# Kernel tuning notes

Hardware: AMD Instinct MI355X
Metric: run time of the kernel (lower is better)

Reference implementation:

```python
import jax, jax.numpy as jnp
import numpy as np

WH, WW = 14, 14
NUM_HEADS = 12
NUM_REL = (2 * WH - 1) * (2 * WW - 1) + 3  # 732


def _gen_rel_pos_index(wh, ww):
    # Faithful numpy port of gen_relative_position_index (static, host-side)
    area = wh * ww
    coords = np.stack(np.meshgrid(np.arange(wh), np.arange(ww), indexing='ij'))  # (2, wh, ww)
    cf = coords.reshape(2, -1)  # (2, area)
    rel = cf[:, :, None] - cf[:, None, :]  # (2, area, area)
    rel = rel.transpose(1, 2, 0).copy()  # (area, area, 2)
    rel[..., 0] += wh - 1
    rel[..., 1] += ww - 1
    rel[..., 0] *= 2 * ww - 1
    nrd = (2 * wh - 1) * (2 * ww - 1) + 3
    idx = np.zeros((area + 1, area + 1), dtype=np.int64)
    idx[1:, 1:] = rel.sum(-1)
    idx[0, 0:] = nrd - 3
    idx[0:, 0] = nrd - 2
    idx[0, 0] = nrd - 1
    return idx


REL_IDX = jnp.asarray(_gen_rel_pos_index(WH, WW))  # (197, 197) int


def setup_inputs() -> dict:
    key = jax.random.key(0)
    k0, k1, k2, k3 = jax.random.split(key, 4)
    B, N, C = 64, WH * WW + 1, 768
    x = jax.random.normal(k0, (B, N, C), jnp.float32)
    qkv_w = jax.random.normal(k1, (3 * C, C), jnp.float32) * 0.02
    q_bias = jnp.zeros((C,), jnp.float32)
    k_bias = jnp.zeros((C,), jnp.float32)  # non-trainable buffer, always zeros
    v_bias = jnp.zeros((C,), jnp.float32)
    rel_table = jax.random.normal(k2, (NUM_REL, NUM_HEADS), jnp.float32) * 0.02
    proj_w = jax.random.normal(k3, (C, C), jnp.float32) * 0.02
    proj_b = jnp.zeros((C,), jnp.float32)
    return {"x": x, "qkv_w": qkv_w, "q_bias": q_bias, "k_bias": k_bias,
            "v_bias": v_bias, "rel_table": rel_table, "proj_w": proj_w, "proj_b": proj_b}


def reference(x, qkv_w, q_bias, k_bias, v_bias, rel_table, proj_w, proj_b):
    B, N, C = x.shape
    H = NUM_HEADS
    D = C // H
    scale = D ** -0.5
    # fused qkv projection with concatenated (q, k(zero), v) bias
    qkv_bias = jnp.concatenate([q_bias, k_bias, v_bias])
    qkv = x @ qkv_w.T + qkv_bias  # (B, N, 3C)
    qkv = qkv.reshape(B, N, 3, H, D).transpose(2, 0, 3, 1, 4)  # (3, B, H, N, D)
    q, k, v = qkv[0], qkv[1], qkv[2]
    # scores + gathered relative position bias
    attn = jnp.einsum('bhnd,bhmd->bhnm', q * scale, k)  # (B, H, N, N)
    rpb = rel_table[REL_IDX].transpose(2, 0, 1)  # (H, N, N)
    attn = jax.nn.softmax(attn + rpb[None], axis=-1)
    out = jnp.einsum('bhnm,bhmd->bhnd', attn, v)  # (B, H, N, D)
    out = out.transpose(0, 2, 1, 3).reshape(B, N, C)
    return out @ proj_w.T + proj_b
```

## Files before the change

kernel.cpp:

```cpp
#include <hip/hip_runtime.h>
#include <math.h>

#define B_   64
#define N_   197
#define C_   768
#define H_   12
#define D_   64
#define BN   12608
#define BN_PAD 12672
#define QKV_ELEMS 9682944
#define SCALE 0.125f
#define STRV 80

typedef unsigned short ushort_t;
using bf16x8  = __attribute__((ext_vector_type(8))) __bf16;
using floatx4 = __attribute__((ext_vector_type(4))) float;
using ushort8 = __attribute__((ext_vector_type(8))) unsigned short;

__device__ __forceinline__ ushort_t f2bf(float f) {
    union { float f; unsigned u; } v; v.f = f;
    unsigned r = v.u + 0x7FFF + ((v.u >> 16) & 1);
    return (ushort_t)(r >> 16);
}

__device__ __forceinline__ void gload_lds16(const void* g, void* l) {
    __builtin_amdgcn_global_load_lds(
        (const __attribute__((address_space(1))) unsigned*)g,
        (__attribute__((address_space(3))) unsigned*)l, 16, 0, 0);
}

__global__ __launch_bounds__(256) void cvt_f32_bf16(
    const float* __restrict__ src, ushort_t* __restrict__ dst, int n4)
{
    int i = blockIdx.x * 256 + threadIdx.x;
    if (i < n4) {
        float4 v = ((const float4*)src)[i];
        ushort4 o;
        o.x = f2bf(v.x); o.y = f2bf(v.y); o.z = f2bf(v.z); o.w = f2bf(v.w);
        ((ushort4*)dst)[i] = o;
    }
}

__global__ __launch_bounds__(256, 4) void qkv_gemm_mfma(
    const ushort_t* __restrict__ xb,
    const ushort_t* __restrict__ wb,
    const float* __restrict__ qb,
    const float* __restrict__ kb,
    const float* __restrict__ vb,
    ushort_t* __restrict__ qkvb)
{
    __shared__ ushort_t lA[128 * 64];
    __shared__ ushort_t lB[128 * 64];
    const int t = threadIdx.x;
    const int w = t >> 6, lane = t & 63;
    const int quad = lane >> 4, li = lane & 15;
    const int wm = w >> 1, wn = w & 1;
    const int o0 = blockIdx.x * 128, m0 = blockIdx.y * 128;

    floatx4 acc[4][4];
#pragma unroll
    for (int i = 0; i < 4; ++i)
#pragma unroll
        for (int j = 0; j < 4; ++j) acc[i][j] = (floatx4)0.f;

    const int rloc = lane >> 3;
    const int gdma = (lane & 7) ^ rloc;
    const int rx   = li & 7;

    for (int kt = 0; kt < 12; ++kt) {
        const int k0 = kt * 64;
#pragma unroll
        for (int s = 0; s < 4; ++s) {
            const int rb = w * 32 + s * 8;
            gload_lds16(xb + ((size_t)(m0 + rb + rloc)) * 768 + k0 + gdma * 8,
                        &lA[rb * 64]);
            gload_lds16(wb + ((size_t)(o0 + rb + rloc)) * 768 + k0 + gdma * 8,
                        &lB[rb * 64]);
        }
        __syncthreads();
#pragma unroll
        for (int kk = 0; kk < 2; ++kk) {
            bf16x8 af[4], bfr[4];
#pragma unroll
            for (int mi = 0; mi < 4; ++mi)
                af[mi] = *(const bf16x8*)
                    &lA[(wm * 64 + mi * 16 + li) * 64 + ((kk * 4 + quad) ^ rx) * 8];
#pragma unroll
            for (int ni = 0; ni < 4; ++ni)
                bfr[ni] = *(const bf16x8*)
                    &lB[(wn * 64 + ni * 16 + li) * 64 + ((kk * 4 + quad) ^ rx) * 8];
#pragma unroll
            for (int mi = 0; mi < 4; ++mi)
#pragma unroll
                for (int ni = 0; ni < 4; ++ni)
                    acc[mi][ni] = __builtin_amdgcn_mfma_f32_16x16x32_bf16(
                        af[mi], bfr[ni], acc[mi][ni], 0, 0, 0);
        }
        __syncthreads();
    }

    const int which = o0 / 768;
    const float* bias = (which == 0) ? qb : ((which == 1) ? kb : vb);
    ushort_t* dst = qkvb + (size_t)which * QKV_ELEMS;
    const float sc = (which == 0) ? SCALE : 1.0f;

#pragma unroll
    for (int mi = 0; mi < 4; ++mi) {
#pragma unroll
        for (int r = 0; r < 4; ++r) {
            const int m = m0 + wm * 64 + mi * 16 + quad * 4 + r;
            if (m < BN) {
                const int b = m / 197, n = m % 197;
#pragma unroll
                for (int ni = 0; ni < 4; ++ni) {
                    const int o  = o0 + wn * 64 + ni * 16 + li;
                    const int ol = o - which * 768;
                    const int h = ol >> 6, d = ol & 63;
                    dst[(((size_t)b * 12 + h) * 197 + n) * 64 + d] =
                        f2bf((acc[mi][ni][r] + bias[ol]) * sc);
                }
            }
        }
    }
}

__global__ __launch_bounds__(256, 4) void attn_mfma(
    const ushort_t* __restrict__ qkvb,
    const float* __restrict__ rel_table,
    ushort_t* __restrict__ aout)
{
    __shared__ ushort_t Qs[64 * 64];
    __shared__ ushort_t Ks[64 * 64];
    __shared__ ushort_t Vt[64 * STRV];
    __shared__ ushort_t Ps[64 * STRV];
    __shared__ float relh[732];

    const int rt = blockIdx.x, bh = blockIdx.y;
    const int h = bh % 12, bb = bh / 12;
    const int t = threadIdx.x;
    const int w = t >> 6, lane = t & 63, quad = lane >> 4, li = lane & 15;
    const size_t base = (size_t)bh * (197 * 64);
    const ushort_t* Qg = qkvb + base;
    const ushort_t* Kg = qkvb + (size_t)QKV_ELEMS + base;
    const ushort_t* Vg = qkvb + (size_t)2 * QKV_ELEMS + base;
    const int r0 = rt * 64;

    for (int i = t; i < 732; i += 256) relh[i] = rel_table[i * 12 + h];

    {
        const int rloc = lane >> 3, g = (lane & 7) ^ rloc;
#pragma unroll
        for (int s = 0; s < 2; ++s) {
            const int rb = (w * 2 + s) * 8;
            gload_lds16(Qg + (size_t)(r0 + rb + rloc) * 64 + g * 8, &Qs[rb * 64]);
        }
    }

    int nrow[4], p14[4], pm[4];
#pragma unroll
    for (int r = 0; r < 4; ++r) {
        const int n = r0 + w * 16 + quad * 4 + r;
        nrow[r] = n;
        const int ne = (n < 197) ? n : 0;
        const int p = (ne > 0) ? ne - 1 : 0;
        p14[r] = p / 14; pm[r] = p % 14;
    }

    float m_run[4], l_run[4];
    floatx4 accO[4];
#pragma unroll
    for (int r = 0; r < 4; ++r) { m_run[r] = -INFINITY; l_run[r] = 0.f; }
#pragma unroll
    for (int dt = 0; dt < 4; ++dt) accO[dt] = (floatx4)0.f;

    __syncthreads();

    bf16x8 aq0, aq1;
    {
        const int rq = w * 16 + li, rxq = rq & 7;
        aq0 = *(const bf16x8*)&Qs[rq * 64 + (quad ^ rxq) * 8];
        aq1 = *(const bf16x8*)&Qs[rq * 64 + ((4 + quad) ^ rxq) * 8];
    }

    for (int cc = 0; cc < 4; ++cc) {
        {
            const int rloc = lane >> 3, g = (lane & 7) ^ rloc;
#pragma unroll
            for (int s = 0; s < 2; ++s) {
                const int rb = (w * 2 + s) * 8;
                gload_lds16(Kg + (size_t)(cc * 64 + rb + rloc) * 64 + g * 8,
                            &Ks[rb * 64]);
            }
        }
        {
            const int c = lane;
            const int mg = cc * 64 + c;
            ushort8 v0, v1;
            if (mg < 197) {
                v0 = *(const ushort8*)(Vg + (size_t)mg * 64 + w * 16);
                v1 = *(const ushort8*)(Vg + (size_t)mg * 64 + w * 16 + 8);
            } else {
                v0 = (ushort8)(unsigned short)0; v1 = v0;
            }
#pragma unroll
            for (int j = 0; j < 8; ++j) Vt[(w * 16 + j) * STRV + c] = v0[j];
#pragma unroll
            for (int j = 0; j < 8; ++j) Vt[(w * 16 + 8 + j) * STRV + c] = v1[j];
        }
        __syncthreads();

        floatx4 sacc[4];
#pragma unroll
        for (int tl = 0; tl < 4; ++tl) {
            const int rk = tl * 16 + li, rxk = rk & 7;
            bf16x8 bk0 = *(const bf16x8*)&Ks[rk * 64 + (quad ^ rxk) * 8];
            bf16x8 bk1 = *(const bf16x8*)&Ks[rk * 64 + ((4 + quad) ^ rxk) * 8];
            floatx4 sa = (floatx4)0.f;
            sa = __builtin_amdgcn_mfma_f32_16x16x32_bf16(aq0, bk0, sa, 0, 0, 0);
            sa = __builtin_amdgcn_mfma_f32_16x16x32_bf16(aq1, bk1, sa, 0, 0, 0);
            sacc[tl] = sa;
        }

#pragma unroll
        for (int tl = 0; tl < 4; ++tl) {
            const int mg = cc * 64 + tl * 16 + li;
            if (mg >= 197) {
#pragma unroll
                for (int r = 0; r < 4; ++r) sacc[tl][r] = -INFINITY;
            } else {
                const int qq = (mg > 0) ? mg - 1 : 0;
                const int q14 = qq / 14, qm = qq % 14;
#pragma unroll
                for (int r = 0; r < 4; ++r) {
                    int idx;
                    const int n0 = (nrow[r] < 197) ? nrow[r] : 0;
                    if (n0 == 0 && mg == 0)      idx = 731;
                    else if (n0 == 0)            idx = 729;
                    else if (mg == 0)            idx = 730;
                    else idx = (p14[r] - q14 + 13) * 27 + (pm[r] - qm + 13);
                    sacc[tl][r] += relh[idx];
                }
            }
        }

#pragma unroll
        for (int r = 0; r < 4; ++r) {
            float mx = fmaxf(fmaxf(sacc[0][r], sacc[1][r]),
                             fmaxf(sacc[2][r], sacc[3][r]));
            mx = fmaxf(mx, __shfl_xor(mx, 1));
            mx = fmaxf(mx, __shfl_xor(mx, 2));
            mx = fmaxf(mx, __shfl_xor(mx, 4));
            mx = fmaxf(mx, __shfl_xor(mx, 8));
            const float mnew = fmaxf(m_run[r], mx);
            const float alpha = __expf(m_run[r] - mnew);
            m_run[r] = mnew;
            const float p0 = __expf(sacc[0][r] - mnew);
            const float p1 = __expf(sacc[1][r] - mnew);
            const float p2 = __expf(sacc[2][r] - mnew);
            const float p3 = __expf(sacc[3][r] - mnew);
            float rs = p0 + p1 + p2 + p3;
            rs += __shfl_xor(rs, 1);
            rs += __shfl_xor(rs, 2);
            rs += __shfl_xor(rs, 4);
            rs += __shfl_xor(rs, 8);
            l_run[r] = l_run[r] * alpha + rs;
#pragma unroll
            for (int dt = 0; dt < 4; ++dt) accO[dt][r] *= alpha;
            const int prow = w * 16 + quad * 4 + r;
            Ps[prow * STRV +  0 + li] = f2bf(p0);
            Ps[prow * STRV + 16 + li] = f2bf(p1);
            Ps[prow * STRV + 32 + li] = f2bf(p2);
            Ps[prow * STRV + 48 + li] = f2bf(p3);
        }

        {
            const int rp = w * 16 + li;
            bf16x8 pa0 = *(const bf16x8*)&Ps[rp * STRV + 0  + quad * 8];
            bf16x8 pa1 = *(const bf16x8*)&Ps[rp * STRV + 32 + quad * 8];
#pragma unroll
            for (int dt = 0; dt < 4; ++dt) {
                const int rv = dt * 16 + li;
                bf16x8 bv0 = *(const bf16x8*)&Vt[rv * STRV + 0  + quad * 8];
                bf16x8 bv1 = *(const bf16x8*)&Vt[rv * STRV + 32 + quad * 8];
                accO[dt] = __builtin_amdgcn_mfma_f32_16x16x32_bf16(
                    pa0, bv0, accO[dt], 0, 0, 0);
                accO[dt] = __builtin_amdgcn_mfma_f32_16x16x32_bf16(
                    pa1, bv1, accO[dt], 0, 0, 0);
            }
        }
        __syncthreads();
    }

#pragma unroll
    for (int r = 0; r < 4; ++r) {
        const int n = nrow[r];
        if (n < 197) {
            const float inv = 1.0f / l_run[r];
            ushort_t* op = aout + ((size_t)(bb * 197 + n)) * 768 + h * 64;
#pragma unroll
            for (int dt = 0; dt < 4; ++dt)
                op[dt * 16 + li] = f2bf(accO[dt][r] * inv);
        }
    }
}

__global__ __launch_bounds__(256, 4) void proj_gemm_mfma(
    const ushort_t* __restrict__ ab,
    const ushort_t* __restrict__ wb,
    const float* __restrict__ bias,
    float* __restrict__ out)
{
    __shared__ ushort_t lA[128 * 64];
    __shared__ ushort_t lB[128 * 64];
    const int t = threadIdx.x;
    const int w = t >> 6, lane = t & 63;
    const int quad = lane >> 4, li = lane & 15;
    const int wm = w >> 1, wn = w & 1;
    const int o0 = blockIdx.x * 128, m0 = blockIdx.y * 128;

    floatx4 acc[4][4];
#pragma unroll
    for (int i = 0; i < 4; ++i)
#pragma unroll
        for (int j = 0; j < 4; ++j) acc[i][j] = (floatx4)0.f;

    const int rloc = lane >> 3;
    const int gdma = (lane & 7) ^ rloc;
    const int rx   = li & 7;

    for (int kt = 0; kt < 12; ++kt) {
        const int k0 = kt * 64;
#pragma unroll
        for (int s = 0; s < 4; ++s) {
            const int rb = w * 32 + s * 8;
            gload_lds16(ab + ((size_t)(m0 + rb + rloc)) * 768 + k0 + gdma * 8,
                        &lA[rb * 64]);
            gload_lds16(wb + ((size_t)(o0 + rb + rloc)) * 768 + k0 + gdma * 8,
                        &lB[rb * 64]);
        }
        __syncthreads();
#pragma unroll
        for (int kk = 0; kk < 2; ++kk) {
            bf16x8 af[4], bfr[4];
#pragma unroll
            for (int mi = 0; mi < 4; ++mi)
                af[mi] = *(const bf16x8*)
                    &lA[(wm * 64 + mi * 16 + li) * 64 + ((kk * 4 + quad) ^ rx) * 8];
#pragma unroll
            for (int ni = 0; ni < 4; ++ni)
                bfr[ni] = *(const bf16x8*)
                    &lB[(wn * 64 + ni * 16 + li) * 64 + ((kk * 4 + quad) ^ rx) * 8];
#pragma unroll
            for (int mi = 0; mi < 4; ++mi)
#pragma unroll
                for (int ni = 0; ni < 4; ++ni)
                    acc[mi][ni] = __builtin_amdgcn_mfma_f32_16x16x32_bf16(
                        af[mi], bfr[ni], acc[mi][ni], 0, 0, 0);
        }
        __syncthreads();
    }

#pragma unroll
    for (int mi = 0; mi < 4; ++mi) {
#pragma unroll
        for (int r = 0; r < 4; ++r) {
            const int m = m0 + wm * 64 + mi * 16 + quad * 4 + r;
            if (m < BN) {
                float* op = out + (size_t)m * 768;
#pragma unroll
                for (int ni = 0; ni < 4; ++ni) {
                    const int o = o0 + wn * 64 + ni * 16 + li;
                    op[o] = acc[mi][ni][r] + bias[o];
                }
            }
        }
    }
}

extern "C" void kernel_launch(void* const* d_in, const int* in_sizes, int n_in,
                              void* d_out, int out_size, void* d_ws, size_t ws_size,
                              hipStream_t stream)
{
    const float* x         = (const float*)d_in[0];
    const float* qkv_w     = (const float*)d_in[1];
    const float* q_bias    = (const float*)d_in[2];
    const float* k_bias    = (const float*)d_in[3];
    const float* v_bias    = (const float*)d_in[4];
    const float* rel_table = (const float*)d_in[5];
    const float* proj_w    = (const float*)d_in[6];
    const float* proj_b    = (const float*)d_in[7];
    float* out = (float*)d_out;

    char* ws = (char*)d_ws;
    ushort_t* qkvb  = (ushort_t*)ws;
    ushort_t* xb    = (ushort_t*)(ws + 58097664);
    ushort_t* aoutb = xb;
    ushort_t* wb    = (ushort_t*)(ws + 77561856);
    ushort_t* pwb   = (ushort_t*)(ws + 81100800);

    cvt_f32_bf16<<<(2420736 + 255) / 256, 256, 0, stream>>>(x, xb, 2420736);
    cvt_f32_bf16<<<(442368 + 255) / 256, 256, 0, stream>>>(qkv_w, wb, 442368);
    cvt_f32_bf16<<<(147456 + 255) / 256, 256, 0, stream>>>(proj_w, pwb, 147456);

    dim3 g1(18, 99);
    qkv_gemm_mfma<<<g1, 256, 0, stream>>>(xb, wb, q_bias, k_bias, v_bias, qkvb);

    dim3 g2(4, 768);
    attn_mfma<<<g2, 256, 0, stream>>>(qkvb, rel_table, aoutb);

    dim3 g3(6, 99);
    proj_gemm_mfma<<<g3, 256, 0, stream>>>(aoutb, pwb, proj_b, out);
}
```

Baseline: 253.3 us.

## Use 256x256 double-buffered ping-pong MFMA GEMM core for QKV and projection

Replaces the 128x128 single-buffered GEMM loops in both the QKV and output projection kernels with a shared 256x256-tile core using 8 waves, double-buffered LDS with direct global-to-LDS loads, and a hand-interleaved schedule of partial loads, barriers and MFMA quarters with raised wave priority. The aim is to overlap global loads with MFMA work and raise arithmetic intensity per tile. In exchange it uses 128 KB of LDS per block, so occupancy drops, and the grid becomes coarse (150 blocks for the projection), which risks underfilling the GPU.

```diff
diff --git a/kernel.cpp b/kernel.cpp
--- a/kernel.cpp
+++ b/kernel.cpp
@@ -41,7 +41,148 @@
     }
 }
 
-__global__ __launch_bounds__(256, 4) void qkv_gemm_mfma(
+
+template<int H>
+__device__ __forceinline__ void lda_half(const ushort_t* src,
+    int wm, int li, int quad, int rx, bf16x8 (&aR)[2][4])
+{
+#pragma unroll
+    for (int kk = 0; kk < 2; ++kk)
+#pragma unroll
+        for (int mi = 0; mi < 4; ++mi)
+            aR[kk][mi] = *(const bf16x8*)&src[
+                (wm*128 + H*64 + mi*16 + li)*64 + (((kk*4+quad)^rx)*8)];
+}
+
+template<int NH>
+__device__ __forceinline__ void ldb_half(const ushort_t* src,
+    int wn, int li, int quad, int rx, bf16x8 (&bR)[2][2][2])
+{
+#pragma unroll
+    for (int kk = 0; kk < 2; ++kk)
+#pragma unroll
+        for (int ni = 0; ni < 2; ++ni)
+            bR[NH][kk][ni] = *(const bf16x8*)&src[
+                (wn*64 + NH*32 + ni*16 + li)*64 + (((kk*4+quad)^rx)*8)];
+}
+
+template<int MH, int NH>
+__device__ __forceinline__ void mm_q(const bf16x8 (&aR)[2][4],
+    const bf16x8 (&bR)[2][2][2], floatx4 (&acc)[8][4])
+{
+#pragma unroll
+    for (int mi = 0; mi < 4; ++mi)
+#pragma unroll
+        for (int ni = 0; ni < 2; ++ni)
+#pragma unroll
+            for (int kk = 0; kk < 2; ++kk)
+                acc[MH*4+mi][NH*2+ni] = __builtin_amdgcn_mfma_f32_16x16x32_bf16(
+                    aR[kk][mi], bR[NH][kk][ni], acc[MH*4+mi][NH*2+ni], 0, 0, 0);
+}
+
+#define BARM()  __builtin_amdgcn_s_barrier()
+#define LGK0()  do { asm volatile("s_waitcnt lgkmcnt(0)" ::: "memory"); \
+                     __builtin_amdgcn_sched_barrier(0); } while (0)
+#define VMW2()  asm volatile("s_waitcnt vmcnt(2)" ::: "memory")
+#define VMW0()  asm volatile("s_waitcnt vmcnt(0)" ::: "memory")
+
+__device__ __forceinline__ void gemm256_core(
+    const ushort_t* __restrict__ Ag, const ushort_t* __restrict__ Bg,
+    const int m0, const int o0, const int maxArow, floatx4 (&acc)[8][4])
+{
+    __shared__ ushort_t lds[65536];
+    const int t = threadIdx.x;
+    const int w = t >> 6, lane = t & 63;
+    const int quad = lane >> 4, li = lane & 15;
+    const int wm = w >> 2, wn = w & 3;
+    const int rx = li & 7;
+    const int r8 = lane >> 3;
+    const int g8 = (lane & 7) ^ r8;
+    const int ldw = w * 512;
+
+    ushort_t* const As0 = lds;
+    ushort_t* const As1 = lds + 16384;
+    ushort_t* const Bs0 = lds + 32768;
+    ushort_t* const Bs1 = lds + 49152;
+
+#pragma unroll
+    for (int i = 0; i < 8; ++i)
+#pragma unroll
+        for (int j = 0; j < 4; ++j) acc[i][j] = (floatx4)0.f;
+
+    const ushort_t* aB[4]; const ushort_t* bB[4];
+#pragma unroll
+    for (int qa = 0; qa < 4; ++qa) {
+        int ra = m0 + qa*64 + w*8 + r8; if (ra > maxArow) ra = maxArow;
+        aB[qa] = Ag + (size_t)ra * 768 + g8*8;
+        bB[qa] = Bg + (size_t)(o0 + qa*64 + w*8 + r8) * 768 + g8*8;
+    }
+
+#define STG(base_, kt_, dst_, qa_) \
+    gload_lds16((base_)[qa_] + (kt_)*64, (dst_) + (qa_)*4096 + ldw)
+
+    STG(aB, 0, As0, 0); STG(aB, 0, As0, 1); STG(aB, 0, As0, 2); STG(aB, 0, As0, 3);
+    STG(bB, 0, Bs0, 0); STG(bB, 0, Bs0, 1); STG(bB, 0, Bs0, 2); STG(bB, 0, Bs0, 3);
+    STG(aB, 1, As1, 0); STG(aB, 1, As1, 2);
+    VMW2(); BARM();
+
+    bf16x8 aR[2][4];
+    bf16x8 bR[2][2][2];
+
+#pragma unroll 1
+    for (int it = 0; it < 6; ++it) {
+        const int tb  = 2 * it;
+        const int kt1 = tb + 1;
+        const int kt2 = (tb + 2 < 12) ? tb + 2 : 11;
+        const int kt3 = (tb + 3 < 12) ? tb + 3 : 11;
+        lda_half<0>(As0, wm, li, quad, rx, aR);
+        ldb_half<0>(Bs0, wn, li, quad, rx, bR);
+        STG(aB, kt1, As1, 1); STG(aB, kt1, As1, 3);
+        BARM(); LGK0();
+        __builtin_amdgcn_s_setprio(1); mm_q<0,0>(aR, bR, acc); __builtin_amdgcn_s_setprio(0);
+        BARM();
+        ldb_half<1>(Bs0, wn, li, quad, rx, bR);
+        STG(bB, kt1, Bs1, 0); STG(bB, kt1, Bs1, 1);
+        BARM(); LGK0();
+        __builtin_amdgcn_s_setprio(1); mm_q<0,1>(aR, bR, acc); __builtin_amdgcn_s_setprio(0);
+        BARM();
+        lda_half<1>(As0, wm, li, quad, rx, aR);
+        STG(bB, kt1, Bs1, 2); STG(bB, kt1, Bs1, 3);
+        BARM(); LGK0();
+        __builtin_amdgcn_s_setprio(1); mm_q<1,0>(aR, bR, acc); __builtin_amdgcn_s_setprio(0);
+        BARM();
+        STG(aB, kt2, As0, 0); STG(aB, kt2, As0, 2);
+        BARM(); LGK0();
+        __builtin_amdgcn_s_setprio(1); mm_q<1,1>(aR, bR, acc); __builtin_amdgcn_s_setprio(0);
+        VMW2();
+        BARM();
+        lda_half<0>(As1, wm, li, quad, rx, aR);
+        ldb_half<0>(Bs1, wn, li, quad, rx, bR);
+        STG(aB, kt2, As0, 1); STG(aB, kt2, As0, 3);
+        BARM(); LGK0();
+        __builtin_amdgcn_s_setprio(1); mm_q<0,0>(aR, bR, acc); __builtin_amdgcn_s_setprio(0);
+        BARM();
+        ldb_half<1>(Bs1, wn, li, quad, rx, bR);
+        STG(bB, kt2, Bs0, 0); STG(bB, kt2, Bs0, 1);
+        BARM(); LGK0();
+        __builtin_amdgcn_s_setprio(1); mm_q<0,1>(aR, bR, acc); __builtin_amdgcn_s_setprio(0);
+        BARM();
+        lda_half<1>(As1, wm, li, quad, rx, aR);
+        STG(bB, kt2, Bs0, 2); STG(bB, kt2, Bs0, 3);
+        BARM(); LGK0();
+        __builtin_amdgcn_s_setprio(1); mm_q<1,0>(aR, bR, acc); __builtin_amdgcn_s_setprio(0);
+        BARM();
+        STG(aB, kt3, As1, 0); STG(aB, kt3, As1, 2);
+        BARM(); LGK0();
+        __builtin_amdgcn_s_setprio(1); mm_q<1,1>(aR, bR, acc); __builtin_amdgcn_s_setprio(0);
+        VMW2();
+        BARM();
+    }
+    VMW0();
+#undef STG
+}
+
+__global__ __launch_bounds__(512, 2) void qkv_gemm_mfma(
     const ushort_t* __restrict__ xb,
     const ushort_t* __restrict__ wb,
     const float* __restrict__ qb,
@@ -49,66 +190,25 @@
     const float* __restrict__ vb,
     ushort_t* __restrict__ qkvb)
 {
-    __shared__ ushort_t lA[128 * 64];
-    __shared__ ushort_t lB[128 * 64];
+    const int o0 = blockIdx.x * 256, m0 = blockIdx.y * 256;
+    floatx4 acc[8][4];
+    gemm256_core(xb, wb, m0, o0, BN_PAD - 1, acc);
+
     const int t = threadIdx.x;
     const int w = t >> 6, lane = t & 63;
     const int quad = lane >> 4, li = lane & 15;
-    const int wm = w >> 1, wn = w & 1;
-    const int o0 = blockIdx.x * 128, m0 = blockIdx.y * 128;
-
-    floatx4 acc[4][4];
-#pragma unroll
-    for (int i = 0; i < 4; ++i)
-#pragma unroll
-        for (int j = 0; j < 4; ++j) acc[i][j] = (floatx4)0.f;
-
-    const int rloc = lane >> 3;
-    const int gdma = (lane & 7) ^ rloc;
-    const int rx   = li & 7;
-
-    for (int kt = 0; kt < 12; ++kt) {
-        const int k0 = kt * 64;
-#pragma unroll
-        for (int s = 0; s < 4; ++s) {
-            const int rb = w * 32 + s * 8;
-            gload_lds16(xb + ((size_t)(m0 + rb + rloc)) * 768 + k0 + gdma * 8,
-                        &lA[rb * 64]);
-            gload_lds16(wb + ((size_t)(o0 + rb + rloc)) * 768 + k0 + gdma * 8,
-                        &lB[rb * 64]);
-        }
-        __syncthreads();
-#pragma unroll
-        for (int kk = 0; kk < 2; ++kk) {
-            bf16x8 af[4], bfr[4];
-#pragma unroll
-            for (int mi = 0; mi < 4; ++mi)
-                af[mi] = *(const bf16x8*)
-                    &lA[(wm * 64 + mi * 16 + li) * 64 + ((kk * 4 + quad) ^ rx) * 8];
-#pragma unroll
-            for (int ni = 0; ni < 4; ++ni)
-                bfr[ni] = *(const bf16x8*)
-                    &lB[(wn * 64 + ni * 16 + li) * 64 + ((kk * 4 + quad) ^ rx) * 8];
-#pragma unroll
-            for (int mi = 0; mi < 4; ++mi)
-#pragma unroll
-                for (int ni = 0; ni < 4; ++ni)
-                    acc[mi][ni] = __builtin_amdgcn_mfma_f32_16x16x32_bf16(
-                        af[mi], bfr[ni], acc[mi][ni], 0, 0, 0);
-        }
-        __syncthreads();
-    }
-
-    const int which = o0 / 768;
+    const int wm = w >> 2, wn = w & 3;
+
+    const int which = blockIdx.x / 3;
     const float* bias = (which == 0) ? qb : ((which == 1) ? kb : vb);
     ushort_t* dst = qkvb + (size_t)which * QKV_ELEMS;
     const float sc = (which == 0) ? SCALE : 1.0f;
 
 #pragma unroll
-    for (int mi = 0; mi < 4; ++mi) {
+    for (int mi = 0; mi < 8; ++mi) {
 #pragma unroll
         for (int r = 0; r < 4; ++r) {
-            const int m = m0 + wm * 64 + mi * 16 + quad * 4 + r;
+            const int m = m0 + wm * 128 + mi * 16 + quad * 4 + r;
             if (m < BN) {
                 const int b = m / 197, n = m % 197;
 #pragma unroll
@@ -304,67 +404,26 @@
     }
 }
 
-__global__ __launch_bounds__(256, 4) void proj_gemm_mfma(
+__global__ __launch_bounds__(512, 2) void proj_gemm_mfma(
     const ushort_t* __restrict__ ab,
     const ushort_t* __restrict__ wb,
     const float* __restrict__ bias,
     float* __restrict__ out)
 {
-    __shared__ ushort_t lA[128 * 64];
-    __shared__ ushort_t lB[128 * 64];
+    const int o0 = blockIdx.x * 256, m0 = blockIdx.y * 256;
+    floatx4 acc[8][4];
+    gemm256_core(ab, wb, m0, o0, BN_PAD - 1, acc);
+
     const int t = threadIdx.x;
     const int w = t >> 6, lane = t & 63;
     const int quad = lane >> 4, li = lane & 15;
-    const int wm = w >> 1, wn = w & 1;
-    const int o0 = blockIdx.x * 128, m0 = blockIdx.y * 128;
-
-    floatx4 acc[4][4];
-#pragma unroll
-    for (int i = 0; i < 4; ++i)
-#pragma unroll
-        for (int j = 0; j < 4; ++j) acc[i][j] = (floatx4)0.f;
-
-    const int rloc = lane >> 3;
-    const int gdma = (lane & 7) ^ rloc;
-    const int rx   = li & 7;
-
-    for (int kt = 0; kt < 12; ++kt) {
-        const int k0 = kt * 64;
-#pragma unroll
-        for (int s = 0; s < 4; ++s) {
-            const int rb = w * 32 + s * 8;
-            gload_lds16(ab + ((size_t)(m0 + rb + rloc)) * 768 + k0 + gdma * 8,
-                        &lA[rb * 64]);
-            gload_lds16(wb + ((size_t)(o0 + rb + rloc)) * 768 + k0 + gdma * 8,
-                        &lB[rb * 64]);
-        }
-        __syncthreads();
-#pragma unroll
-        for (int kk = 0; kk < 2; ++kk) {
-            bf16x8 af[4], bfr[4];
-#pragma unroll
-            for (int mi = 0; mi < 4; ++mi)
-                af[mi] = *(const bf16x8*)
-                    &lA[(wm * 64 + mi * 16 + li) * 64 + ((kk * 4 + quad) ^ rx) * 8];
-#pragma unroll
-            for (int ni = 0; ni < 4; ++ni)
-                bfr[ni] = *(const bf16x8*)
-                    &lB[(wn * 64 + ni * 16 + li) * 64 + ((kk * 4 + quad) ^ rx) * 8];
-#pragma unroll
-            for (int mi = 0; mi < 4; ++mi)
-#pragma unroll
-                for (int ni = 0; ni < 4; ++ni)
-                    acc[mi][ni] = __builtin_amdgcn_mfma_f32_16x16x32_bf16(
-                        af[mi], bfr[ni], acc[mi][ni], 0, 0, 0);
-        }
-        __syncthreads();
-    }
-
-#pragma unroll
-    for (int mi = 0; mi < 4; ++mi) {
+    const int wm = w >> 2, wn = w & 3;
+
+#pragma unroll
+    for (int mi = 0; mi < 8; ++mi) {
 #pragma unroll
         for (int r = 0; r < 4; ++r) {
-            const int m = m0 + wm * 64 + mi * 16 + quad * 4 + r;
+            const int m = m0 + wm * 128 + mi * 16 + quad * 4 + r;
             if (m < BN) {
                 float* op = out + (size_t)m * 768;
 #pragma unroll
@@ -402,12 +461,12 @@
     cvt_f32_bf16<<<(442368 + 255) / 256, 256, 0, stream>>>(qkv_w, wb, 442368);
     cvt_f32_bf16<<<(147456 + 255) / 256, 256, 0, stream>>>(proj_w, pwb, 147456);
 
-    dim3 g1(18, 99);
-    qkv_gemm_mfma<<<g1, 256, 0, stream>>>(xb, wb, q_bias, k_bias, v_bias, qkvb);
+    dim3 g1(9, 50);
+    qkv_gemm_mfma<<<g1, 512, 0, stream>>>(xb, wb, q_bias, k_bias, v_bias, qkvb);
 
     dim3 g2(4, 768);
     attn_mfma<<<g2, 256, 0, stream>>>(qkvb, rel_table, aoutb);
 
-    dim3 g3(6, 99);
-    proj_gemm_mfma<<<g3, 256, 0, stream>>>(aoutb, pwb, proj_b, out);
-}
+    dim3 g3(3, 50);
+    proj_gemm_mfma<<<g3, 512, 0, stream>>>(aoutb, pwb, proj_b, out);
+}
```

Result: no change. 248.7 us (-1.8%).
